# Kernel optimization log

Hardware: AMD Instinct MI355X
Metric: run time of the kernel (lower is better)

## Reference

```python
import jax, jax.numpy as jnp
import numpy as np


def setup_inputs() -> dict:
    key = jax.random.key(0)
    k1, k2, k3 = jax.random.split(key, 3)
    b, H, W, T = 2, 24, 24, 24
    c = 512
    n = H * W * T
    x = jax.random.normal(k1, (b, n, c), jnp.float32)
    w_qkv = jax.random.normal(k2, (c, 3 * c), jnp.float32) * 0.02
    w_proj = jax.random.normal(k3, (c, c), jnp.float32) * 0.02
    return {"x": x, "w_qkv": w_qkv, "w_proj": w_proj, "h": H, "w": W, "t": T, "head_num": 8}


def _attn(q, k, v, scale):
    # q,k,v: (B, nh, L, hd). NOTE: original multiplies q by sqrt(head_dim).
    s = jnp.einsum('bnqd,bnkd->bnqk', q * scale, k)
    a = jax.nn.softmax(s, axis=-1)
    return jnp.einsum('bnqk,bnkd->bnqd', a, v)  # (B, nh, L, hd)


def reference(x, w_qkv, w_proj, h, w, t, head_num):
    b, n, c = x.shape
    hd = c // head_num
    scale = float(hd) ** 0.5  # faithful: q * sqrt(head_dim)
    qkv = (x @ w_qkv).reshape(b, h, w, t, 3, head_num, hd)
    q = qkv[..., 0, :, :]  # (b,h,w,t,nh,hd)
    k = qkv[..., 1, :, :]
    v = qkv[..., 2, :, :]

    # axis 1: attention over (h w), batch over (b t)
    def to_hw(a):
        return a.transpose(0, 3, 4, 1, 2, 5).reshape(b * t, head_num, h * w, hd)
    o1 = _attn(to_hw(q), to_hw(k), to_hw(v), scale)
    o1 = o1.reshape(b, t, head_num, h, w, hd).transpose(0, 3, 4, 1, 2, 5)

    # axis 2: attention over (h t), batch over (b w)
    def to_ht(a):
        return a.transpose(0, 2, 4, 1, 3, 5).reshape(b * w, head_num, h * t, hd)
    o2 = _attn(to_ht(q), to_ht(k), to_ht(v), scale)
    o2 = o2.reshape(b, w, head_num, h, t, hd).transpose(0, 3, 1, 4, 2, 5)

    # axis 3: attention over (w t), batch over (b h)
    def to_wt(a):
        return a.transpose(0, 1, 4, 2, 3, 5).reshape(b * h, head_num, w * t, hd)
    o3 = _attn(to_wt(q), to_wt(k), to_wt(v), scale)
    o3 = o3.reshape(b, h, head_num, w, t, hd).transpose(0, 1, 3, 4, 2, 5)

    out = (o1 + o2 + o3).reshape(b, n, c)  # (nh, hd) merged -> c
    return out @ w_proj
```

## Files before the change

kernel.cpp:

```cpp
#include <hip/hip_runtime.h>
#include <math.h>

constexpr int Cc     = 512;
constexpr int NHEAD  = 8;
constexpr int HD     = 64;
constexpr int NTOK   = 13824;
constexpr int BATCH  = 2;
constexpr int M_TOT  = BATCH * NTOK;
constexpr int QKV_LD = 3 * Cc;
constexpr int SEQLEN = 576;
constexpr int NTILE  = SEQLEN / 64;
constexpr int KT     = 16;

#define QSCALE 11.541560327111707f

typedef short s16x8 __attribute__((ext_vector_type(8)));
typedef float f32x4 __attribute__((ext_vector_type(4)));

__device__ __forceinline__ unsigned short f2bf(float f) {
  unsigned u = __float_as_uint(f);
  unsigned r = u + 0x7fffu + ((u >> 16) & 1u);
  return (unsigned short)(r >> 16);
}
__device__ __forceinline__ float bf2f(unsigned short b) {
  return __uint_as_float(((unsigned)b) << 16);
}

template<bool WRITE_LO>
__global__ __launch_bounds__(256)
void conv_a_frag(const float* __restrict__ src, s16x8* __restrict__ dh,
                 s16x8* __restrict__ dl) {
  int g  = blockIdx.x * 256 + threadIdx.x;
  int l  = g & 63;
  int t  = g >> 6;
  int kt = t & (KT - 1);
  int mt = t >> 4;
  const float* p = src + (size_t)(mt * 16 + (l & 15)) * 512 + kt * 32 + (l >> 4) * 8;
  float4 a = *(const float4*)p;
  float4 b = *(const float4*)(p + 4);
  float xs[8] = {a.x, a.y, a.z, a.w, b.x, b.y, b.z, b.w};
  s16x8 h, lo;
#pragma unroll
  for (int j = 0; j < 8; ++j) {
    unsigned short hh = f2bf(xs[j]);
    h[j] = (short)hh;
    if (WRITE_LO) lo[j] = (short)f2bf(xs[j] - bf2f(hh));
  }
  dh[g] = h;
  if (WRITE_LO) dl[g] = lo;
}

template<bool WRITE_LO>
__global__ __launch_bounds__(256)
void conv_b_frag(const float* __restrict__ src, s16x8* __restrict__ dh,
                 s16x8* __restrict__ dl, int N) {
  int g  = blockIdx.x * 256 + threadIdx.x;
  int l  = g & 63;
  int t  = g >> 6;
  int kt = t & (KT - 1);
  int nt = t >> 4;
  int col  = nt * 16 + (l & 15);
  int row0 = kt * 32 + (l >> 4) * 8;
  s16x8 h, lo;
#pragma unroll
  for (int j = 0; j < 8; ++j) {
    float v = src[(size_t)(row0 + j) * N + col];
    unsigned short hh = f2bf(v);
    h[j] = (short)hh;
    if (WRITE_LO) lo[j] = (short)f2bf(v - bf2f(hh));
  }
  dh[g] = h;
  if (WRITE_LO) dl[g] = lo;
}

__global__ __launch_bounds__(256)
void conv_o_frag(const unsigned short* __restrict__ O0,
                 const unsigned short* __restrict__ O1,
                 const unsigned short* __restrict__ O2,
                 s16x8* __restrict__ dh) {
  int g  = blockIdx.x * 256 + threadIdx.x;
  int l  = g & 63;
  int t  = g >> 6;
  int kt = t & (KT - 1);
  int mt = t >> 4;
  int row = mt * 16 + (l & 15);
  int c0  = kt * 32 + (l >> 4) * 8;
  int head = c0 >> 6;
  size_t off = ((size_t)head * M_TOT + row) * 64 + (c0 & 63);
  s16x8 a = *(const s16x8*)(O0 + off);
  s16x8 b = *(const s16x8*)(O1 + off);
  s16x8 c = *(const s16x8*)(O2 + off);
  s16x8 h;
#pragma unroll
  for (int j = 0; j < 8; ++j) {
    float v = bf2f((unsigned short)a[j]) + bf2f((unsigned short)b[j]) +
              bf2f((unsigned short)c[j]);
    h[j] = (short)f2bf(v);
  }
  dh[g] = h;
}

template<int SPLIT, int MODE>
__global__ __launch_bounds__(256)
void gemm_frag(const s16x8* __restrict__ Ah, const s16x8* __restrict__ Al,
               const s16x8* __restrict__ Bh, const s16x8* __restrict__ Bl,
               float* __restrict__ C,
               unsigned short* __restrict__ p0, unsigned short* __restrict__ p1,
               unsigned short* __restrict__ p2, unsigned short* __restrict__ p3,
               int nbx, int n0, int N_ld, int ntoff) {
  int nwg = gridDim.x;
  int cpx = nwg >> 3;
  int bid = blockIdx.x;
  int swz = (bid & 7) * cpx + (bid >> 3);
  int bx = swz % nbx;
  int by = swz / nbx;

  int tid  = threadIdx.x;
  int lane = tid & 63;
  int w    = tid >> 6;
  int wm   = w & 1;
  int wn   = w >> 1;
  int mt0  = by * 8 + wm * 4;
  int ntG  = ntoff + bx * 8 + wn * 4;

  const f32x4 fz = {0.0f, 0.0f, 0.0f, 0.0f};
  f32x4 acc[4][4];
#pragma unroll
  for (int mi = 0; mi < 4; ++mi)
#pragma unroll
    for (int ni = 0; ni < 4; ++ni) acc[mi][ni] = fz;

#pragma unroll 2
  for (int kt = 0; kt < KT; ++kt) {
    s16x8 ah[4], bh[4];
#pragma unroll
    for (int mi = 0; mi < 4; ++mi)
      ah[mi] = Ah[(size_t)(((mt0 + mi) * KT + kt) * 64 + lane)];
#pragma unroll
    for (int ni = 0; ni < 4; ++ni)
      bh[ni] = Bh[(size_t)(((ntG + ni) * KT + kt) * 64 + lane)];

    if constexpr (SPLIT == 3) {
      s16x8 al[4], bl[4];
#pragma unroll
      for (int mi = 0; mi < 4; ++mi)
        al[mi] = Al[(size_t)(((mt0 + mi) * KT + kt) * 64 + lane)];
#pragma unroll
      for (int ni = 0; ni < 4; ++ni)
        bl[ni] = Bl[(size_t)(((ntG + ni) * KT + kt) * 64 + lane)];
#pragma unroll
      for (int mi = 0; mi < 4; ++mi)
#pragma unroll
        for (int ni = 0; ni < 4; ++ni) {
          acc[mi][ni] = __builtin_amdgcn_mfma_f32_16x16x32_bf16(ah[mi], bh[ni], acc[mi][ni], 0, 0, 0);
          acc[mi][ni] = __builtin_amdgcn_mfma_f32_16x16x32_bf16(al[mi], bh[ni], acc[mi][ni], 0, 0, 0);
          acc[mi][ni] = __builtin_amdgcn_mfma_f32_16x16x32_bf16(ah[mi], bl[ni], acc[mi][ni], 0, 0, 0);
        }
    } else {
#pragma unroll
      for (int mi = 0; mi < 4; ++mi)
#pragma unroll
        for (int ni = 0; ni < 4; ++ni)
          acc[mi][ni] = __builtin_amdgcn_mfma_f32_16x16x32_bf16(ah[mi], bh[ni], acc[mi][ni], 0, 0, 0);
    }
  }

  int lg = lane >> 4, l15 = lane & 15;
  if constexpr (MODE == 0) {
#pragma unroll
    for (int mi = 0; mi < 4; ++mi) {
#pragma unroll
      for (int r = 0; r < 4; ++r) {
        int row = by * 128 + wm * 64 + mi * 16 + lg * 4 + r;
        float* cp = C + (size_t)row * N_ld + n0 + bx * 128 + wn * 64 + l15;
#pragma unroll
        for (int ni = 0; ni < 4; ++ni) cp[ni * 16] = acc[mi][ni][r];
      }
    }
  } else {
    int colb = bx * 128 + wn * 64;
    int head = (colb >> 6) & 7;
    const bool isq = (MODE == 1) && (colb < 512);
    unsigned short* Hp;
    unsigned short* Lp = nullptr;
    float sc = 1.0f;
    if (MODE == 2)      { Hp = p0; }
    else if (isq)       { Hp = p0; Lp = p1; sc = QSCALE; }
    else                { Hp = p2; Lp = p3; }
    size_t hb = (size_t)head * ((size_t)M_TOT * 64);
#pragma unroll
    for (int mi = 0; mi < 4; ++mi) {
#pragma unroll
      for (int r = 0; r < 4; ++r) {
        int row = by * 128 + wm * 64 + mi * 16 + lg * 4 + r;
        size_t base = hb + (size_t)row * 64;
#pragma unroll
        for (int ni = 0; ni < 4; ++ni) {
          int d = ni * 16 + l15;
          float v = acc[mi][ni][r] * sc;
          unsigned short hh = f2bf(v);
          Hp[base + d] = hh;
          if (MODE == 1) Lp[base + d] = f2bf(v - bf2f(hh));
        }
      }
    }
  }
}

__global__ __launch_bounds__(256, 2)
void attn_def(const unsigned short* __restrict__ QH, const unsigned short* __restrict__ QL,
              const unsigned short* __restrict__ KH, const unsigned short* __restrict__ KL,
              const unsigned short* __restrict__ VH, unsigned short* __restrict__ Op,
              int str1, int str2, int strE) {
  __shared__ __align__(16) unsigned short L[16384];

  int bi = (blockIdx.x & 7) * 432 + (blockIdx.x >> 3);
  const int qt   = bi % NTILE;
  const int head = (bi / NTILE) & 7;
  const int be   = bi / (NTILE * NHEAD);
  const int bb   = be / 24;
  const int e    = be % 24;

  const int tid  = threadIdx.x;
  const int w    = tid >> 6;
  const int lane = tid & 63;
  const int l15  = lane & 15;
  const int lg   = lane >> 4;

  const size_t base_tok = (size_t)bb * NTOK + (size_t)e * strE;
  const size_t pb = ((size_t)head * M_TOT + base_tok) * 64;
  const unsigned short* qhp = QH + pb;
  const unsigned short* qlp = QL + pb;
  const unsigned short* khp = KH + pb;
  const unsigned short* klp = KL + pb;
  const unsigned short* vhp = VH + pb;

  s16x8 qh[2], ql[2];
  {
    int s  = qt * 64 + w * 16 + l15;
    size_t no = (size_t)((s / 24) * str1 + (s % 24) * str2) * 64 + lg * 8;
    qh[0] = *(const s16x8*)(qhp + no);
    qh[1] = *(const s16x8*)(qhp + no + 32);
    ql[0] = *(const s16x8*)(qlp + no);
    ql[1] = *(const s16x8*)(qlp + no + 32);
  }

  const f32x4 fz = {0.0f, 0.0f, 0.0f, 0.0f};
  f32x4 S[NTILE][4];

  const int cc = tid & 7;
  const int r0 = tid >> 3;

  s16x8 kr[2][2], lr[2][2];
#pragma unroll
  for (int hf = 0; hf < 2; ++hf) {
    int s = r0 + hf * 32;
    size_t no = (size_t)((s / 24) * str1 + (s % 24) * str2) * 64 + cc * 8;
    kr[0][hf] = *(const s16x8*)(khp + no);
    lr[0][hf] = *(const s16x8*)(klp + no);
  }

#pragma unroll
  for (int t = 0; t < NTILE; ++t) {
    const int b = t & 1;
#pragma unroll
    for (int hf = 0; hf < 2; ++hf) {
      int r = r0 + hf * 32;
      int off = b * 4096 + (r << 6) + ((cc ^ (r & 7)) << 3);
      *(s16x8*)&L[off]        = kr[b][hf];
      *(s16x8*)&L[8192 + off] = lr[b][hf];
    }
    if (t < NTILE - 1) {
#pragma unroll
      for (int hf = 0; hf < 2; ++hf) {
        int s = (t + 1) * 64 + r0 + hf * 32;
        size_t no = (size_t)((s / 24) * str1 + (s % 24) * str2) * 64 + cc * 8;
        kr[b ^ 1][hf] = *(const s16x8*)(khp + no);
        lr[b ^ 1][hf] = *(const s16x8*)(klp + no);
      }
    }
    asm volatile("s_waitcnt lgkmcnt(0)" ::: "memory");
    __builtin_amdgcn_s_barrier();
    __builtin_amdgcn_s_setprio(1);
#pragma unroll
    for (int n = 0; n < 4; ++n) S[t][n] = fz;
#pragma unroll
    for (int ks = 0; ks < 2; ++ks) {
#pragma unroll
      for (int n = 0; n < 4; ++n) {
        int krow = (n << 4) + l15;
        int off  = b * 4096 + (krow << 6) + (((ks * 4 + lg) ^ (krow & 7)) << 3);
        s16x8 kfh = *(const s16x8*)&L[off];
        s16x8 kfl = *(const s16x8*)&L[8192 + off];
        S[t][n] = __builtin_amdgcn_mfma_f32_16x16x32_bf16(qh[ks], kfh, S[t][n], 0, 0, 0);
        S[t][n] = __builtin_amdgcn_mfma_f32_16x16x32_bf16(ql[ks], kfh, S[t][n], 0, 0, 0);
        S[t][n] = __builtin_amdgcn_mfma_f32_16x16x32_bf16(qh[ks], kfl, S[t][n], 0, 0, 0);
      }
    }
    __builtin_amdgcn_s_setprio(0);
  }

  const int rp = (tid & 31) * 2;
  const int cb = tid >> 5;
  s16x8 vr[2][2];
#pragma unroll
  for (int pp = 0; pp < 2; ++pp) {
    int s = rp + pp;
    size_t no = (size_t)((s / 24) * str1 + (s % 24) * str2) * 64 + cb * 8;
    vr[0][pp] = *(const s16x8*)(vhp + no);
  }

  float linv[4];
#pragma unroll
  for (int rr = 0; rr < 4; ++rr) {
    float m0 = S[0][0][rr];
#pragma unroll
    for (int t = 0; t < NTILE; ++t)
#pragma unroll
      for (int n = 0; n < 4; ++n) m0 = fmaxf(m0, S[t][n][rr]);
    m0 = fmaxf(m0, __shfl_xor(m0, 1));
    m0 = fmaxf(m0, __shfl_xor(m0, 2));
    m0 = fmaxf(m0, __shfl_xor(m0, 4));
    m0 = fmaxf(m0, __shfl_xor(m0, 8));
    float ts = 0.0f;
#pragma unroll
    for (int t = 0; t < NTILE; ++t)
#pragma unroll
      for (int n = 0; n < 4; ++n) {
        float p = exp2f(S[t][n][rr] - m0);
        S[t][n][rr] = p;
        ts += p;
      }
    ts += __shfl_xor(ts, 1);
    ts += __shfl_xor(ts, 2);
    ts += __shfl_xor(ts, 4);
    ts += __shfl_xor(ts, 8);
    linv[rr] = 1.0f / ts;
  }

  __syncthreads();

  f32x4 Ov[4];
#pragma unroll
  for (int n = 0; n < 4; ++n) Ov[n] = fz;
  const int prow = (w << 4) + (lg << 2);

#pragma unroll
  for (int t = 0; t < NTILE; ++t) {
    const int b = t & 1;
#pragma unroll
    for (int j = 0; j < 8; ++j) {
      int d = cb * 8 + j;
      unsigned pk = (unsigned)(unsigned short)vr[b][0][j] |
                    ((unsigned)(unsigned short)vr[b][1][j] << 16);
      int off = b * 4096 + (d << 6) + (((rp >> 3) ^ (d & 7)) << 3) + (rp & 7);
      *(unsigned*)&L[off] = pk;
    }
    if (t < NTILE - 1) {
#pragma unroll
      for (int pp = 0; pp < 2; ++pp) {
        int s = (t + 1) * 64 + rp + pp;
        size_t no = (size_t)((s / 24) * str1 + (s % 24) * str2) * 64 + cb * 8;
        vr[b ^ 1][pp] = *(const s16x8*)(vhp + no);
      }
    }
#pragma unroll
    for (int n = 0; n < 4; ++n) {
      int col = (n << 4) + l15;
#pragma unroll
      for (int rr = 0; rr < 4; ++rr) {
        int row = prow + rr;
        int off = 8192 + (row << 6) + (((col >> 3) ^ (row & 7)) << 3) + (col & 7);
        L[off] = f2bf(S[t][n][rr]);
      }
    }
    asm volatile("s_waitcnt lgkmcnt(0)" ::: "memory");
    __builtin_amdgcn_s_barrier();
    __builtin_amdgcn_s_setprio(1);
#pragma unroll
    for (int ks = 0; ks < 2; ++ks) {
      int arow = (w << 4) + l15;
      int aoff = 8192 + (arow << 6) + (((ks * 4 + lg) ^ (arow & 7)) << 3);
      s16x8 pa = *(const s16x8*)&L[aoff];
#pragma unroll
      for (int n = 0; n < 4; ++n) {
        int vrow = (n << 4) + l15;
        int voff = b * 4096 + (vrow << 6) + (((ks * 4 + lg) ^ (vrow & 7)) << 3);
        s16x8 vb = *(const s16x8*)&L[voff];
        Ov[n] = __builtin_amdgcn_mfma_f32_16x16x32_bf16(pa, vb, Ov[n], 0, 0, 0);
      }
    }
    __builtin_amdgcn_s_setprio(0);
  }

  __syncthreads();
#pragma unroll
  for (int n = 0; n < 4; ++n) {
#pragma unroll
    for (int rr = 0; rr < 4; ++rr) {
      int row = prow + rr;
      int col = (n << 4) + l15;
      L[row * 72 + col] = f2bf(Ov[n][rr] * linv[rr]);
    }
  }
  __syncthreads();
#pragma unroll
  for (int it = 0; it < 2; ++it) {
    int q   = it * 256 + tid;
    int row = q >> 3, c8 = q & 7;
    s16x8 ov = *(const s16x8*)&L[row * 72 + c8 * 8];
    int s = qt * 64 + row;
    size_t no = (size_t)((s / 24) * str1 + (s % 24) * str2) * 64 + c8 * 8;
    *(s16x8*)(Op + pb + no) = ov;
  }
}

extern "C" void kernel_launch(void* const* d_in, const int* in_sizes, int n_in,
                              void* d_out, int out_size, void* d_ws, size_t ws_size,
                              hipStream_t stream) {
  (void)in_sizes; (void)n_in; (void)out_size; (void)ws_size;
  const float* x      = (const float*)d_in[0];
  const float* w_qkv  = (const float*)d_in[1];
  const float* w_proj = (const float*)d_in[2];
  float* out = (float*)d_out;

  char* ws = (char*)d_ws;
  constexpr size_t PL_E = (size_t)NHEAD * M_TOT * 64;
  constexpr size_t PL_B = PL_E * 2;
  unsigned short* QHp = (unsigned short*)ws;
  unsigned short* QLp = QHp + PL_E;
  unsigned short* KHp = QHp + 2 * PL_E;
  unsigned short* KLp = QHp + 3 * PL_E;
  unsigned short* VHp = QHp + 4 * PL_E;
  unsigned short* O0  = QHp + 5 * PL_E;
  unsigned short* O1  = QHp + 6 * PL_E;
  unsigned short* O2  = QHp + 7 * PL_E;
  s16x8* Bh = (s16x8*)(ws + 8 * PL_B);
  s16x8* Bl = (s16x8*)(ws + 8 * PL_B + 1572864);
  s16x8* Ah = (s16x8*)(ws + 5 * PL_B);
  s16x8* Al = (s16x8*)(ws + 6 * PL_B);
  s16x8* Oh = (s16x8*)ws;
  s16x8* Ph = (s16x8*)(ws + PL_B);

  unsigned short* nu = nullptr;

  conv_a_frag<true><<<M_TOT * 64 / 256, 256, 0, stream>>>(x, Ah, Al);
  conv_b_frag<true><<<KT * (QKV_LD / 16) * 64 / 256, 256, 0, stream>>>(w_qkv, Bh, Bl, QKV_LD);

  gemm_frag<3, 1><<<(M_TOT / 128) * 8, 256, 0, stream>>>(
      Ah, Al, Bh, Bl, nullptr, QHp, QLp, KHp, KLp, 8, 0, 0, 0);
  gemm_frag<1, 2><<<(M_TOT / 128) * 4, 256, 0, stream>>>(
      Ah, nullptr, Bh, nullptr, nullptr, VHp, nu, nu, nu, 4, 0, 0, 64);

  attn_def<<<48 * NHEAD * NTILE, 256, 0, stream>>>(QHp, QLp, KHp, KLp, VHp, O0, 576, 24, 1);
  attn_def<<<48 * NHEAD * NTILE, 256, 0, stream>>>(QHp, QLp, KHp, KLp, VHp, O1, 576, 1, 24);
  attn_def<<<48 * NHEAD * NTILE, 256, 0, stream>>>(QHp, QLp, KHp, KLp, VHp, O2, 24, 1, 576);

  conv_o_frag<<<M_TOT * 64 / 256, 256, 0, stream>>>(O0, O1, O2, Oh);
  conv_b_frag<false><<<KT * (Cc / 16) * 64 / 256, 256, 0, stream>>>(w_proj, Ph, nullptr, Cc);
  gemm_frag<1, 0><<<(M_TOT / 128) * 4, 256, 0, stream>>>(
      Oh, nullptr, Ph, nullptr, out, nu, nu, nu, nu, 4, 0, Cc, 0);
}
```

Measured before the change: 661.9 us.

## Fuse three axial attention launches into one online-softmax flash kernel

```diff
diff --git a/kernel.cpp b/kernel.cpp
--- a/kernel.cpp
+++ b/kernel.cpp
@@ -11,11 +11,14 @@
 constexpr int SEQLEN = 576;
 constexpr int NTILE  = SEQLEN / 64;
 constexpr int KT     = 16;
+constexpr size_t PL_E = (size_t)NHEAD * M_TOT * 64;
 
 #define QSCALE 11.541560327111707f
 
 typedef short s16x8 __attribute__((ext_vector_type(8)));
+typedef short s16x4 __attribute__((ext_vector_type(4)));
 typedef float f32x4 __attribute__((ext_vector_type(4)));
+typedef unsigned u32x2 __attribute__((ext_vector_type(2)));
 
 __device__ __forceinline__ unsigned short f2bf(float f) {
   unsigned u = __float_as_uint(f);
@@ -24,6 +27,15 @@
 }
 __device__ __forceinline__ float bf2f(unsigned short b) {
   return __uint_as_float(((unsigned)b) << 16);
+}
+__device__ __forceinline__ unsigned cvtpk_bf16(float lo, float hi) {
+  unsigned r;
+  asm("v_cvt_pk_bf16_f32 %0, %1, %2" : "=v"(r) : "v"(lo), "v"(hi));
+  return r;
+}
+__device__ __forceinline__ void pv_mfma16(f32x4& d, s16x4 a, s16x4 b) {
+  asm("s_nop 1\n\tv_mfma_f32_16x16x16_bf16 %0, %1, %2, %0"
+      : "+v"(d) : "v"(a), "v"(b));
 }
 
 template<bool WRITE_LO>
@@ -207,14 +219,19 @@
   }
 }
 
-__global__ __launch_bounds__(256, 2)
-void attn_def(const unsigned short* __restrict__ QH, const unsigned short* __restrict__ QL,
-              const unsigned short* __restrict__ KH, const unsigned short* __restrict__ KL,
-              const unsigned short* __restrict__ VH, unsigned short* __restrict__ Op,
-              int str1, int str2, int strE) {
-  __shared__ __align__(16) unsigned short L[16384];
-
-  int bi = (blockIdx.x & 7) * 432 + (blockIdx.x >> 3);
+__global__ __launch_bounds__(256, 3)
+void attn_fused(const unsigned short* __restrict__ QH, const unsigned short* __restrict__ QL,
+                const unsigned short* __restrict__ KH, const unsigned short* __restrict__ KL,
+                const unsigned short* __restrict__ VH, unsigned short* __restrict__ Oall) {
+  __shared__ __align__(16) unsigned short L[24576];
+
+  const int p  = blockIdx.x / 3456;
+  const int rr_ = blockIdx.x % 3456;
+  const int bi = (rr_ & 7) * 432 + (rr_ >> 3);
+  const int str1 = (p == 2) ? 24 : 576;
+  const int str2 = (p == 0) ? 24 : 1;
+  const int strE = (p == 0) ? 1 : (p == 1 ? 24 : 576);
+
   const int qt   = bi % NTILE;
   const int head = (bi / NTILE) & 7;
   const int be   = bi / (NTILE * NHEAD);
@@ -234,6 +251,7 @@
   const unsigned short* khp = KH + pb;
   const unsigned short* klp = KL + pb;
   const unsigned short* vhp = VH + pb;
+  unsigned short* Op = Oall + (size_t)p * PL_E;
 
   s16x8 qh[2], ql[2];
   {
@@ -245,13 +263,12 @@
     ql[1] = *(const s16x8*)(qlp + no + 32);
   }
 
-  const f32x4 fz = {0.0f, 0.0f, 0.0f, 0.0f};
-  f32x4 S[NTILE][4];
-
   const int cc = tid & 7;
   const int r0 = tid >> 3;
-
-  s16x8 kr[2][2], lr[2][2];
+  const int rp = (tid & 31) * 2;
+  const int cb = tid >> 5;
+
+  s16x8 kr[2][2], lr[2][2], vr[2][2];
 #pragma unroll
   for (int hf = 0; hf < 2; ++hf) {
     int s = r0 + hf * 32;
@@ -259,6 +276,18 @@
     kr[0][hf] = *(const s16x8*)(khp + no);
     lr[0][hf] = *(const s16x8*)(klp + no);
   }
+#pragma unroll
+  for (int pp = 0; pp < 2; ++pp) {
+    int s = rp + pp;
+    size_t no = (size_t)((s / 24) * str1 + (s % 24) * str2) * 64 + cb * 8;
+    vr[0][pp] = *(const s16x8*)(vhp + no);
+  }
+
+  const f32x4 fz = {0.0f, 0.0f, 0.0f, 0.0f};
+  f32x4 Ov[4];
+#pragma unroll
+  for (int n = 0; n < 4; ++n) Ov[n] = fz;
+  float m_run = -1e30f, l_run = 0.0f;
 
 #pragma unroll
   for (int t = 0; t < NTILE; ++t) {
@@ -270,6 +299,14 @@
       *(s16x8*)&L[off]        = kr[b][hf];
       *(s16x8*)&L[8192 + off] = lr[b][hf];
     }
+#pragma unroll
+    for (int j = 0; j < 8; ++j) {
+      int d = cb * 8 + j;
+      unsigned pk = (unsigned)(unsigned short)vr[b][0][j] |
+                    ((unsigned)(unsigned short)vr[b][1][j] << 16);
+      int off = 16384 + b * 4096 + (d << 6) + (((rp >> 3) ^ (d & 7)) << 3) + (rp & 7);
+      *(unsigned*)&L[off] = pk;
+    }
     if (t < NTILE - 1) {
 #pragma unroll
       for (int hf = 0; hf < 2; ++hf) {
@@ -278,12 +315,20 @@
         kr[b ^ 1][hf] = *(const s16x8*)(khp + no);
         lr[b ^ 1][hf] = *(const s16x8*)(klp + no);
       }
+#pragma unroll
+      for (int pp = 0; pp < 2; ++pp) {
+        int s = (t + 1) * 64 + rp + pp;
+        size_t no = (size_t)((s / 24) * str1 + (s % 24) * str2) * 64 + cb * 8;
+        vr[b ^ 1][pp] = *(const s16x8*)(vhp + no);
+      }
     }
     asm volatile("s_waitcnt lgkmcnt(0)" ::: "memory");
     __builtin_amdgcn_s_barrier();
+
+    f32x4 Sv[4];
+#pragma unroll
+    for (int n = 0; n < 4; ++n) Sv[n] = fz;
     __builtin_amdgcn_s_setprio(1);
-#pragma unroll
-    for (int n = 0; n < 4; ++n) S[t][n] = fz;
 #pragma unroll
     for (int ks = 0; ks < 2; ++ks) {
 #pragma unroll
@@ -292,116 +337,86 @@
         int off  = b * 4096 + (krow << 6) + (((ks * 4 + lg) ^ (krow & 7)) << 3);
         s16x8 kfh = *(const s16x8*)&L[off];
         s16x8 kfl = *(const s16x8*)&L[8192 + off];
-        S[t][n] = __builtin_amdgcn_mfma_f32_16x16x32_bf16(qh[ks], kfh, S[t][n], 0, 0, 0);
-        S[t][n] = __builtin_amdgcn_mfma_f32_16x16x32_bf16(ql[ks], kfh, S[t][n], 0, 0, 0);
-        S[t][n] = __builtin_amdgcn_mfma_f32_16x16x32_bf16(qh[ks], kfl, S[t][n], 0, 0, 0);
+        Sv[n] = __builtin_amdgcn_mfma_f32_16x16x32_bf16(kfh, qh[ks], Sv[n], 0, 0, 0);
+        Sv[n] = __builtin_amdgcn_mfma_f32_16x16x32_bf16(kfl, qh[ks], Sv[n], 0, 0, 0);
+        Sv[n] = __builtin_amdgcn_mfma_f32_16x16x32_bf16(kfh, ql[ks], Sv[n], 0, 0, 0);
       }
     }
     __builtin_amdgcn_s_setprio(0);
-  }
-
-  const int rp = (tid & 31) * 2;
-  const int cb = tid >> 5;
-  s16x8 vr[2][2];
-#pragma unroll
-  for (int pp = 0; pp < 2; ++pp) {
-    int s = rp + pp;
-    size_t no = (size_t)((s / 24) * str1 + (s % 24) * str2) * 64 + cb * 8;
-    vr[0][pp] = *(const s16x8*)(vhp + no);
-  }
-
-  float linv[4];
-#pragma unroll
-  for (int rr = 0; rr < 4; ++rr) {
-    float m0 = S[0][0][rr];
-#pragma unroll
-    for (int t = 0; t < NTILE; ++t)
-#pragma unroll
-      for (int n = 0; n < 4; ++n) m0 = fmaxf(m0, S[t][n][rr]);
-    m0 = fmaxf(m0, __shfl_xor(m0, 1));
-    m0 = fmaxf(m0, __shfl_xor(m0, 2));
-    m0 = fmaxf(m0, __shfl_xor(m0, 4));
-    m0 = fmaxf(m0, __shfl_xor(m0, 8));
+
+    float vmax = Sv[0][0];
+#pragma unroll
+    for (int n = 0; n < 4; ++n)
+#pragma unroll
+      for (int r = 0; r < 4; ++r) vmax = fmaxf(vmax, Sv[n][r]);
+    vmax = fmaxf(vmax, __shfl_xor(vmax, 16));
+    vmax = fmaxf(vmax, __shfl_xor(vmax, 32));
+    if (!__all(vmax <= m_run + 8.0f)) {
+      float mn = fmaxf(m_run, vmax);
+      float alpha = exp2f(m_run - mn);
+      m_run = mn;
+      l_run *= alpha;
+      float a0 = __shfl(alpha, lg * 4 + 0);
+      float a1 = __shfl(alpha, lg * 4 + 1);
+      float a2 = __shfl(alpha, lg * 4 + 2);
+      float a3 = __shfl(alpha, lg * 4 + 3);
+#pragma unroll
+      for (int n = 0; n < 4; ++n) {
+        Ov[n][0] *= a0; Ov[n][1] *= a1; Ov[n][2] *= a2; Ov[n][3] *= a3;
+      }
+    }
     float ts = 0.0f;
 #pragma unroll
-    for (int t = 0; t < NTILE; ++t)
-#pragma unroll
-      for (int n = 0; n < 4; ++n) {
-        float p = exp2f(S[t][n][rr] - m0);
-        S[t][n][rr] = p;
-        ts += p;
-      }
-    ts += __shfl_xor(ts, 1);
-    ts += __shfl_xor(ts, 2);
-    ts += __shfl_xor(ts, 4);
-    ts += __shfl_xor(ts, 8);
-    linv[rr] = 1.0f / ts;
-  }
-
+    for (int n = 0; n < 4; ++n)
+#pragma unroll
+      for (int r = 0; r < 4; ++r) {
+        float pv = exp2f(Sv[n][r] - m_run);
+        Sv[n][r] = pv;
+        ts += pv;
+      }
+    ts += __shfl_xor(ts, 16);
+    ts += __shfl_xor(ts, 32);
+    l_run += ts;
+
+    s16x4 pa[4];
+#pragma unroll
+    for (int n = 0; n < 4; ++n) {
+      u32x2 t2;
+      t2[0] = cvtpk_bf16(Sv[n][0], Sv[n][1]);
+      t2[1] = cvtpk_bf16(Sv[n][2], Sv[n][3]);
+      pa[n] = __builtin_bit_cast(s16x4, t2);
+    }
+#pragma unroll
+    for (int n = 0; n < 4; ++n) {
+      int d = n * 16 + l15;
+      int dbase = 16384 + b * 4096 + (d << 6);
+      int dx = d & 7;
+#pragma unroll
+      for (int kb = 0; kb < 4; ++kb) {
+        int chunk = 2 * kb + (lg >> 1);
+        int off = dbase + ((chunk ^ dx) << 3) + ((lg & 1) << 2);
+        s16x4 vb = *(const s16x4*)&L[off];
+        pv_mfma16(Ov[n], pa[kb], vb);
+      }
+    }
+    __builtin_amdgcn_sched_barrier(0);
+  }
+
+  asm volatile("s_nop 7\n\ts_nop 7" :::);
+  float linv = 1.0f / l_run;
+  float l0 = __shfl(linv, lg * 4 + 0);
+  float l1 = __shfl(linv, lg * 4 + 1);
+  float l2 = __shfl(linv, lg * 4 + 2);
+  float l3 = __shfl(linv, lg * 4 + 3);
   __syncthreads();
-
-  f32x4 Ov[4];
-#pragma unroll
-  for (int n = 0; n < 4; ++n) Ov[n] = fz;
   const int prow = (w << 4) + (lg << 2);
-
-#pragma unroll
-  for (int t = 0; t < NTILE; ++t) {
-    const int b = t & 1;
-#pragma unroll
-    for (int j = 0; j < 8; ++j) {
-      int d = cb * 8 + j;
-      unsigned pk = (unsigned)(unsigned short)vr[b][0][j] |
-                    ((unsigned)(unsigned short)vr[b][1][j] << 16);
-      int off = b * 4096 + (d << 6) + (((rp >> 3) ^ (d & 7)) << 3) + (rp & 7);
-      *(unsigned*)&L[off] = pk;
-    }
-    if (t < NTILE - 1) {
-#pragma unroll
-      for (int pp = 0; pp < 2; ++pp) {
-        int s = (t + 1) * 64 + rp + pp;
-        size_t no = (size_t)((s / 24) * str1 + (s % 24) * str2) * 64 + cb * 8;
-        vr[b ^ 1][pp] = *(const s16x8*)(vhp + no);
-      }
-    }
-#pragma unroll
-    for (int n = 0; n < 4; ++n) {
-      int col = (n << 4) + l15;
-#pragma unroll
-      for (int rr = 0; rr < 4; ++rr) {
-        int row = prow + rr;
-        int off = 8192 + (row << 6) + (((col >> 3) ^ (row & 7)) << 3) + (col & 7);
-        L[off] = f2bf(S[t][n][rr]);
-      }
-    }
-    asm volatile("s_waitcnt lgkmcnt(0)" ::: "memory");
-    __builtin_amdgcn_s_barrier();
-    __builtin_amdgcn_s_setprio(1);
-#pragma unroll
-    for (int ks = 0; ks < 2; ++ks) {
-      int arow = (w << 4) + l15;
-      int aoff = 8192 + (arow << 6) + (((ks * 4 + lg) ^ (arow & 7)) << 3);
-      s16x8 pa = *(const s16x8*)&L[aoff];
-#pragma unroll
-      for (int n = 0; n < 4; ++n) {
-        int vrow = (n << 4) + l15;
-        int voff = b * 4096 + (vrow << 6) + (((ks * 4 + lg) ^ (vrow & 7)) << 3);
-        s16x8 vb = *(const s16x8*)&L[voff];
-        Ov[n] = __builtin_amdgcn_mfma_f32_16x16x32_bf16(pa, vb, Ov[n], 0, 0, 0);
-      }
-    }
-    __builtin_amdgcn_s_setprio(0);
-  }
-
-  __syncthreads();
 #pragma unroll
   for (int n = 0; n < 4; ++n) {
-#pragma unroll
-    for (int rr = 0; rr < 4; ++rr) {
-      int row = prow + rr;
-      int col = (n << 4) + l15;
-      L[row * 72 + col] = f2bf(Ov[n][rr] * linv[rr]);
-    }
+    int col = (n << 4) + l15;
+    L[(prow + 0) * 72 + col] = f2bf(Ov[n][0] * l0);
+    L[(prow + 1) * 72 + col] = f2bf(Ov[n][1] * l1);
+    L[(prow + 2) * 72 + col] = f2bf(Ov[n][2] * l2);
+    L[(prow + 3) * 72 + col] = f2bf(Ov[n][3] * l3);
   }
   __syncthreads();
 #pragma unroll
@@ -425,7 +440,6 @@
   float* out = (float*)d_out;
 
   char* ws = (char*)d_ws;
-  constexpr size_t PL_E = (size_t)NHEAD * M_TOT * 64;
   constexpr size_t PL_B = PL_E * 2;
   unsigned short* QHp = (unsigned short*)ws;
   unsigned short* QLp = QHp + PL_E;
@@ -452,9 +466,7 @@
   gemm_frag<1, 2><<<(M_TOT / 128) * 4, 256, 0, stream>>>(
       Ah, nullptr, Bh, nullptr, nullptr, VHp, nu, nu, nu, 4, 0, 0, 64);
 
-  attn_def<<<48 * NHEAD * NTILE, 256, 0, stream>>>(QHp, QLp, KHp, KLp, VHp, O0, 576, 24, 1);
-  attn_def<<<48 * NHEAD * NTILE, 256, 0, stream>>>(QHp, QLp, KHp, KLp, VHp, O1, 576, 1, 24);
-  attn_def<<<48 * NHEAD * NTILE, 256, 0, stream>>>(QHp, QLp, KHp, KLp, VHp, O2, 24, 1, 576);
+  attn_fused<<<3 * 48 * NHEAD * NTILE, 256, 0, stream>>>(QHp, QLp, KHp, KLp, VHp, O0);
 
   conv_o_frag<<<M_TOT * 64 / 256, 256, 0, stream>>>(O0, O1, O2, Oh);
   conv_b_frag<false><<<KT * (Cc / 16) * 64 / 256, 256, 0, stream>>>(w_proj, Ph, nullptr, Cc);
```

Result: faster. 577.1 us (-12.8%).
